# Kernel optimization log

Measured on AMD Instinct MI355X. Metric: run time of the kernel, lower is better.

Reference implementation:

```python
import jax, jax.numpy as jnp
import numpy as np

HID = 64
ENC_T = 20
DEC_T = 30


def lstm_cell(x, h, c, W_ih, W_hh, b_ih, b_hh):
    # PyTorch LSTMCell gate order: i, f, g, o
    gates = x @ W_ih.T + h @ W_hh.T + b_ih + b_hh  # [B, 4*HID]
    i, f, g, o = jnp.split(gates, 4, axis=-1)
    c_new = jax.nn.sigmoid(f) * c + jax.nn.sigmoid(i) * jnp.tanh(g)
    h_new = jax.nn.sigmoid(o) * jnp.tanh(c_new)
    return h_new, c_new


def setup_inputs() -> dict:
    key = jax.random.key(0)
    ks = jax.random.split(key, 11)
    B = 65536
    s_enc = 1.0 / np.sqrt(HID)
    u = lambda k, shape: jax.random.uniform(k, shape, jnp.float32, -s_enc, s_enc)
    return {
        "train_traj": jax.random.normal(ks[0], (B, ENC_T, 2), jnp.float32),
        "W_ih_enc": u(ks[1], (4 * HID, 2)),
        "W_hh_enc": u(ks[2], (4 * HID, HID)),
        "b_ih_enc": u(ks[3], (4 * HID,)),
        "b_hh_enc": u(ks[4], (4 * HID,)),
        "W_ih_dec": u(ks[5], (4 * HID, HID)),
        "W_hh_dec": u(ks[6], (4 * HID, HID)),
        "b_ih_dec": u(ks[7], (4 * HID,)),
        "b_hh_dec": u(ks[8], (4 * HID,)),
        "W_pos": u(ks[9], (2, HID)),
        "b_pos": u(ks[10], (2,)),
    }


def reference(train_traj, W_ih_enc, W_hh_enc, b_ih_enc, b_hh_enc,
              W_ih_dec, W_hh_dec, b_ih_dec, b_hh_dec, W_pos, b_pos):
    B = train_traj.shape[0]
    h0 = jnp.zeros((B, HID), train_traj.dtype)
    c0 = jnp.zeros((B, HID), train_traj.dtype)

    # Encoder: scan over the 20 time steps
    def enc_step(carry, x_t):
        h, c = carry
        h, c = lstm_cell(x_t, h, c, W_ih_enc, W_hh_enc, b_ih_enc, b_hh_enc)
        return (h, c), None

    xs = jnp.transpose(train_traj, (1, 0, 2))  # [T, B, 2]
    (h, c), _ = jax.lax.scan(enc_step, (h0, c0), xs)

    # Decoder: feed h back in as the input for 30 steps
    def dec_step(carry, _):
        h, c = carry
        h_new, c_new = lstm_cell(h, h, c, W_ih_dec, W_hh_dec, b_ih_dec, b_hh_dec)
        out = h_new @ W_pos.T + b_pos  # [B, 2]
        return (h_new, c_new), out

    (_, _), outs = jax.lax.scan(dec_step, (h, c), None, length=DEC_T)
    return jnp.transpose(outs, (1, 0, 2))  # [B, 30, 2]
```

## Files before the change

### kernel.cpp

```cpp
#include <hip/hip_runtime.h>

#define HID   64
#define ENC_T 20
#define DEC_T 30
#define ROWS  32
#define HS    72

typedef _Float16 f16;
typedef _Float16 f16x8 __attribute__((ext_vector_type(8)));
typedef _Float16 f16x4 __attribute__((ext_vector_type(4)));
typedef float  f32x4  __attribute__((ext_vector_type(4)));
typedef float  f32x2  __attribute__((ext_vector_type(2)));
typedef unsigned int   uint_t;

#if __has_builtin(__builtin_amdgcn_exp2f)
#define EXP2F(x) __builtin_amdgcn_exp2f(x)
#else
#define EXP2F(x) exp2f(x)
#endif
#if __has_builtin(__builtin_amdgcn_rcpf)
#define RCPF(x) __builtin_amdgcn_rcpf(x)
#else
#define RCPF(x) (1.0f / (x))
#endif

#define L2E 1.4426950408889634f

__device__ __forceinline__ f32x4 batch_inv4(float D0, float D1, float D2, float D3) {
    float m01 = D0 * D1;
    float m23 = D2 * D3;
    float r   = RCPF(m01 * m23);
    float r01 = r * m23;
    float r23 = r * m01;
    f32x4 o;
    o[0] = r01 * D1;
    o[1] = r01 * D0;
    o[2] = r23 * D3;
    o[3] = r23 * D2;
    return o;
}

__device__ __forceinline__ f16x8 load8h(const float* __restrict__ p, float s) {
    f16x8 r;
    #pragma unroll
    for (int u = 0; u < 8; ++u) r[u] = (f16)(p[u] * s);
    return r;
}

__global__ __launch_bounds__(256, 2)
void lstm_seq2seq(const float* __restrict__ traj,
                  const float* __restrict__ WihE, const float* __restrict__ WhhE,
                  const float* __restrict__ bihE, const float* __restrict__ bhhE,
                  const float* __restrict__ WihD, const float* __restrict__ WhhD,
                  const float* __restrict__ bihD, const float* __restrict__ bhhD,
                  const float* __restrict__ Wpos, const float* __restrict__ bpos,
                  float* __restrict__ out)
{
    __shared__ __align__(16) f16   sH[2][ROWS * HS];
    __shared__ __align__(16) f16x4 sXh[ROWS * ENC_T + ENC_T];
    __shared__ __align__(16) float sP[2][ROWS * 8];

    const int tid  = threadIdx.x;
    const int w    = tid >> 6;
    const int lane = tid & 63;
    const int col  = lane & 15;
    const int quad = lane >> 4;
    const int wg   = blockIdx.x;

    const float gsc[4] = { L2E, L2E, 2.0f * L2E, L2E };

    {
        const float* src = traj + (size_t)wg * (ROWS * ENC_T * 2);
        for (int p = tid; p < ROWS * ENC_T; p += 256) {
            f32x2 xp = *(const f32x2*)(src + 2 * p);
            f16 xh0 = (f16)xp[0], xh1 = (f16)xp[1];
            f16x4 v;
            v[0] = xh0; v[1] = xh1;
            v[2] = (f16)(xp[0] - (float)xh0);
            v[3] = (f16)(xp[1] - (float)xh1);
            sXh[p] = v;
        }
        if (tid < ENC_T) {
            f16x4 zz = {};
            sXh[ROWS * ENC_T + tid] = zz;
        }
    }
    {
        uint_t* hz = (uint_t*)&sH[0][0];
        for (int j = tid; j < ROWS * HS / 2; j += 256) hz[j] = 0;
    }

    f16x8 bw[4][3];
    #pragma unroll
    for (int j = 0; j < 4; ++j) {
        int g = 64 * j + 16 * w + col;
        #pragma unroll
        for (int kb = 0; kb < 2; ++kb)
            bw[j][kb] = load8h(WhhE + g * 64 + kb * 32 + quad * 8, gsc[j]);
        float w0 = WihE[g * 2 + 0] * gsc[j];
        float w1 = WihE[g * 2 + 1] * gsc[j];
        float bs = (bihE[g] + bhhE[g]) * gsc[j];
        f16 w0h = (f16)w0, w1h = (f16)w1, bh = (f16)bs;
        f16 w0l = (f16)(w0 - (float)w0h);
        f16 w1l = (f16)(w1 - (float)w1h);
        f16 bl  = (f16)(bs - (float)bh);
        f16x8 a2 = {};
        if (quad == 0) {
            a2[0] = w0h; a2[1] = w1h; a2[2] = w0l; a2[3] = w1l; a2[4] = bh; a2[5] = bl;
        }
        bw[j][2] = a2;
    }

    const uint_t onesd = (quad == 0) ? 0x3C003C00u : 0u;
    const int xbase0 = (quad == 0) ? (col      * ENC_T) : (ROWS * ENC_T);
    const int xbase1 = (quad == 0) ? ((col+16) * ENC_T) : (ROWS * ENC_T);
    const f32x4 z4 = { 0.f, 0.f, 0.f, 0.f };

    float c[2][4] = {{0.f,0.f,0.f,0.f},{0.f,0.f,0.f,0.f}};
    int buf = 0;

    __syncthreads();

    for (int t = 0; t < ENC_T; ++t) {
        #pragma unroll
        for (int g = 0; g < 2; ++g) {
            const int colg = col + 16 * g;
            union { f16x4 v; uint_t d[2]; } xfu;
            xfu.v = sXh[(g ? xbase1 : xbase0) + t];
            union { f16x8 v; uint_t d[4]; } b2u;
            b2u.d[0] = xfu.d[0];
            b2u.d[1] = xfu.d[1];
            b2u.d[2] = onesd;
            b2u.d[3] = 0;
            f16x8 b0 = *(const f16x8*)&sH[buf][colg * HS +  0 + quad * 8];
            f16x8 b1 = *(const f16x8*)&sH[buf][colg * HS + 32 + quad * 8];
            f32x4 acc[4];
            #pragma unroll
            for (int j = 0; j < 4; ++j) {
                acc[j] = __builtin_amdgcn_mfma_f32_16x16x32_f16(bw[j][2], b2u.v, z4, 0, 0, 0);
                acc[j] = __builtin_amdgcn_mfma_f32_16x16x32_f16(bw[j][0], b0, acc[j], 0, 0, 0);
                acc[j] = __builtin_amdgcn_mfma_f32_16x16x32_f16(bw[j][1], b1, acc[j], 0, 0, 0);
            }
            float so[4], cnv[4];
            #pragma unroll
            for (int r = 0; r < 4; ++r) {
                float ei = EXP2F(-acc[0][r]);
                float ef = EXP2F(-acc[1][r]);
                float eg = EXP2F(-acc[2][r]);
                float eo = EXP2F(-acc[3][r]);
                f32x4 inv = batch_inv4(1.0f + ei, 1.0f + ef, 1.0f + eg, 1.0f + eo);
                float tg = fmaf(2.0f, inv[2], -1.0f);
                float cn = fmaf(inv[1], c[g][r], inv[0] * tg);
                c[g][r] = cn;
                cnv[r] = cn;
                so[r] = inv[3];
            }
            float Dc[4];
            #pragma unroll
            for (int r = 0; r < 4; ++r) {
                float xs = cnv[r] * (-2.0f * L2E);
                xs = fminf(fmaxf(xs, -30.0f), 30.0f);
                Dc[r] = 1.0f + EXP2F(xs);
            }
            f32x4 invc = batch_inv4(Dc[0], Dc[1], Dc[2], Dc[3]);
            f16x4 hh;
            #pragma unroll
            for (int r = 0; r < 4; ++r) {
                float th = fmaf(2.0f, invc[r], -1.0f);
                float hn = so[r] * th;
                hh[r] = (f16)hn;
            }
            *(f16x4*)&sH[buf ^ 1][colg * HS + 16 * w + quad * 4] = hh;
        }
        __syncthreads();
        buf ^= 1;
    }

    f32x4 bD4[4];
    #pragma unroll
    for (int j = 0; j < 4; ++j) {
        int g = 64 * j + 16 * w + col;
        #pragma unroll
        for (int kb = 0; kb < 2; ++kb) {
            int off = g * 64 + kb * 32 + quad * 8;
            float tmp[8];
            #pragma unroll
            for (int u = 0; u < 8; ++u) tmp[u] = WihD[off + u] + WhhD[off + u];
            bw[j][kb] = load8h(tmp, gsc[j]);
        }
        #pragma unroll
        for (int r = 0; r < 4; ++r) {
            int gr = 64 * j + 16 * w + quad * 4 + r;
            bD4[j][r] = (bihD[gr] + bhhD[gr]) * gsc[j];
        }
    }

    float wpA[4], wpB[4];
    #pragma unroll
    for (int r = 0; r < 4; ++r) {
        int u = 16 * w + quad * 4 + r;
        wpA[r] = Wpos[u];
        wpB[r] = Wpos[64 + u];
    }
    const int   rrow  = w * 8 + (lane >> 1);
    const int   rcomp = lane & 1;
    const float bp    = bpos[rcomp];

    for (int t = 0; t < DEC_T; ++t) {
        #pragma unroll
        for (int g = 0; g < 2; ++g) {
            const int colg = col + 16 * g;
            f16x8 b0 = *(const f16x8*)&sH[buf][colg * HS +  0 + quad * 8];
            f16x8 b1 = *(const f16x8*)&sH[buf][colg * HS + 32 + quad * 8];
            f32x4 acc[4];
            #pragma unroll
            for (int j = 0; j < 4; ++j) {
                acc[j] = __builtin_amdgcn_mfma_f32_16x16x32_f16(bw[j][0], b0, bD4[j], 0, 0, 0);
                acc[j] = __builtin_amdgcn_mfma_f32_16x16x32_f16(bw[j][1], b1, acc[j], 0, 0, 0);
            }
            float so[4], cnv[4];
            #pragma unroll
            for (int r = 0; r < 4; ++r) {
                float ei = EXP2F(-acc[0][r]);
                float ef = EXP2F(-acc[1][r]);
                float eg = EXP2F(-acc[2][r]);
                float eo = EXP2F(-acc[3][r]);
                f32x4 inv = batch_inv4(1.0f + ei, 1.0f + ef, 1.0f + eg, 1.0f + eo);
                float tg = fmaf(2.0f, inv[2], -1.0f);
                float cn = fmaf(inv[1], c[g][r], inv[0] * tg);
                c[g][r] = cn;
                cnv[r] = cn;
                so[r] = inv[3];
            }
            float Dc[4];
            #pragma unroll
            for (int r = 0; r < 4; ++r) {
                float xs = cnv[r] * (-2.0f * L2E);
                xs = fminf(fmaxf(xs, -30.0f), 30.0f);
                Dc[r] = 1.0f + EXP2F(xs);
            }
            f32x4 invc = batch_inv4(Dc[0], Dc[1], Dc[2], Dc[3]);
            f16x4 hh;
            float p0 = 0.f, p1 = 0.f;
            #pragma unroll
            for (int r = 0; r < 4; ++r) {
                float th = fmaf(2.0f, invc[r], -1.0f);
                float hn = so[r] * th;
                p0 = fmaf(hn, wpA[r], p0);
                p1 = fmaf(hn, wpB[r], p1);
                hh[r] = (f16)hn;
            }
            *(f16x4*)&sH[buf ^ 1][colg * HS + 16 * w + quad * 4] = hh;
            p0 += __shfl_xor(p0, 16, 64);
            p0 += __shfl_xor(p0, 32, 64);
            p1 += __shfl_xor(p1, 16, 64);
            p1 += __shfl_xor(p1, 32, 64);
            if (quad == 0) {
                sP[buf ^ 1][colg * 8 + 0 + w] = p0;
                sP[buf ^ 1][colg * 8 + 4 + w] = p1;
            }
        }
        __syncthreads();
        buf ^= 1;
        if (lane < 16) {
            f32x4 v = *(const f32x4*)&sP[buf][rrow * 8 + rcomp * 4];
            float p = (v[0] + v[1]) + (v[2] + v[3]) + bp;
            out[(size_t)(wg * ROWS + rrow) * (DEC_T * 2) + t * 2 + rcomp] = p;
        }
    }
}

extern "C" void kernel_launch(void* const* d_in, const int* in_sizes, int n_in,
                              void* d_out, int out_size, void* d_ws, size_t ws_size,
                              hipStream_t stream) {
    const float* traj = (const float*)d_in[0];
    const float* WihE = (const float*)d_in[1];
    const float* WhhE = (const float*)d_in[2];
    const float* bihE = (const float*)d_in[3];
    const float* bhhE = (const float*)d_in[4];
    const float* WihD = (const float*)d_in[5];
    const float* WhhD = (const float*)d_in[6];
    const float* bihD = (const float*)d_in[7];
    const float* bhhD = (const float*)d_in[8];
    const float* Wpos = (const float*)d_in[9];
    const float* bpos = (const float*)d_in[10];
    float* out = (float*)d_out;

    const int B = in_sizes[0] / (ENC_T * 2);
    const int grid = B / ROWS;

    lstm_seq2seq<<<grid, 256, 0, stream>>>(traj, WihE, WhhE, bihE, bhhE,
                                           WihD, WhhD, bihD, bhhD, Wpos, bpos, out);
}
```

Measured before the change: 316.3 us.

## Compute position projection with MFMA from shared h and pack gate math into float2

The decoder's output projection h·W_pos^T, previously computed with per-lane FMAs, cross-lane shuffles and a shared-memory reduction buffer, is now done by wave 0 with four MFMAs over the h tile already loaded from shared memory. W_pos is split into hi/lo fp16 parts for accuracy. Each step's projection is issued one step late, with a final epilogue for the last step. The gate nonlinearities are also rewritten on float2 vectors to encourage packed FP32 instructions. This removes the shuffles, the sP buffer and the per-step reduction after the barrier, at the cost of extra MFMA work on wave 0 only, which unbalances the waves.

```diff
diff --git a/kernel.cpp b/kernel.cpp
--- a/kernel.cpp
+++ b/kernel.cpp
@@ -26,6 +26,24 @@
 
 #define L2E 1.4426950408889634f
 
+__device__ __forceinline__ f32x2 exp2_2(f32x2 x) {
+    f32x2 r; r[0] = EXP2F(x[0]); r[1] = EXP2F(x[1]); return r;
+}
+__device__ __forceinline__ void batch_inv4_pk(f32x2 D0, f32x2 D1, f32x2 D2, f32x2 D3,
+                                              f32x2& i0, f32x2& i1, f32x2& i2, f32x2& i3) {
+    f32x2 m01 = D0 * D1;
+    f32x2 m23 = D2 * D3;
+    f32x2 p   = m01 * m23;
+    f32x2 r;
+    r[0] = RCPF(p[0]);
+    r[1] = RCPF(p[1]);
+    f32x2 r01 = r * m23;
+    f32x2 r23 = r * m01;
+    i0 = r01 * D1;
+    i1 = r01 * D0;
+    i2 = r23 * D3;
+    i3 = r23 * D2;
+}
 __device__ __forceinline__ f32x4 batch_inv4(float D0, float D1, float D2, float D3) {
     float m01 = D0 * D1;
     float m23 = D2 * D3;
@@ -58,7 +76,6 @@
 {
     __shared__ __align__(16) f16   sH[2][ROWS * HS];
     __shared__ __align__(16) f16x4 sXh[ROWS * ENC_T + ENC_T];
-    __shared__ __align__(16) float sP[2][ROWS * 8];
 
     const int tid  = threadIdx.x;
     const int w    = tid >> 6;
@@ -116,7 +133,12 @@
     const int xbase1 = (quad == 0) ? ((col+16) * ENC_T) : (ROWS * ENC_T);
     const f32x4 z4 = { 0.f, 0.f, 0.f, 0.f };
 
-    float c[2][4] = {{0.f,0.f,0.f,0.f},{0.f,0.f,0.f,0.f}};
+    const f32x2 one2  = { 1.f, 1.f };
+    const f32x2 two2  = { 2.f, 2.f };
+    const f32x2 mone2 = { -1.f, -1.f };
+    const f32x2 msc2  = { -2.f * L2E, -2.f * L2E };
+
+    f32x2 c2[2][2] = {{{0.f,0.f},{0.f,0.f}},{{0.f,0.f},{0.f,0.f}}};
     int buf = 0;
 
     __syncthreads();
@@ -141,34 +163,39 @@
                 acc[j] = __builtin_amdgcn_mfma_f32_16x16x32_f16(bw[j][0], b0, acc[j], 0, 0, 0);
                 acc[j] = __builtin_amdgcn_mfma_f32_16x16x32_f16(bw[j][1], b1, acc[j], 0, 0, 0);
             }
-            float so[4], cnv[4];
-            #pragma unroll
-            for (int r = 0; r < 4; ++r) {
-                float ei = EXP2F(-acc[0][r]);
-                float ef = EXP2F(-acc[1][r]);
-                float eg = EXP2F(-acc[2][r]);
-                float eo = EXP2F(-acc[3][r]);
-                f32x4 inv = batch_inv4(1.0f + ei, 1.0f + ef, 1.0f + eg, 1.0f + eo);
-                float tg = fmaf(2.0f, inv[2], -1.0f);
-                float cn = fmaf(inv[1], c[g][r], inv[0] * tg);
-                c[g][r] = cn;
-                cnv[r] = cn;
-                so[r] = inv[3];
+            f32x2 so2[2], cn2[2];
+            #pragma unroll
+            for (int rp = 0; rp < 2; ++rp) {
+                f32x2 a0 = { acc[0][2*rp], acc[0][2*rp+1] };
+                f32x2 a1 = { acc[1][2*rp], acc[1][2*rp+1] };
+                f32x2 a2v = { acc[2][2*rp], acc[2][2*rp+1] };
+                f32x2 a3 = { acc[3][2*rp], acc[3][2*rp+1] };
+                f32x2 i0, i1, i2, i3;
+                batch_inv4_pk(exp2_2(-a0) + one2, exp2_2(-a1) + one2,
+                              exp2_2(-a2v) + one2, exp2_2(-a3) + one2,
+                              i0, i1, i2, i3);
+                f32x2 tg = __builtin_elementwise_fma(two2, i2, mone2);
+                f32x2 cn = __builtin_elementwise_fma(i1, c2[g][rp], i0 * tg);
+                c2[g][rp] = cn;
+                cn2[rp] = cn;
+                so2[rp] = i3;
             }
             float Dc[4];
             #pragma unroll
-            for (int r = 0; r < 4; ++r) {
-                float xs = cnv[r] * (-2.0f * L2E);
-                xs = fminf(fmaxf(xs, -30.0f), 30.0f);
-                Dc[r] = 1.0f + EXP2F(xs);
+            for (int rp = 0; rp < 2; ++rp) {
+                f32x2 xs = cn2[rp] * msc2;
+                Dc[2*rp+0] = 1.f + EXP2F(fminf(fmaxf(xs[0], -30.f), 30.f));
+                Dc[2*rp+1] = 1.f + EXP2F(fminf(fmaxf(xs[1], -30.f), 30.f));
             }
             f32x4 invc = batch_inv4(Dc[0], Dc[1], Dc[2], Dc[3]);
             f16x4 hh;
             #pragma unroll
-            for (int r = 0; r < 4; ++r) {
-                float th = fmaf(2.0f, invc[r], -1.0f);
-                float hn = so[r] * th;
-                hh[r] = (f16)hn;
+            for (int rp = 0; rp < 2; ++rp) {
+                f32x2 ic = { invc[2*rp], invc[2*rp+1] };
+                f32x2 th = __builtin_elementwise_fma(two2, ic, mone2);
+                f32x2 hn = so2[rp] * th;
+                hh[2*rp+0] = (f16)hn[0];
+                hh[2*rp+1] = (f16)hn[1];
             }
             *(f16x4*)&sH[buf ^ 1][colg * HS + 16 * w + quad * 4] = hh;
         }
@@ -195,16 +222,23 @@
         }
     }
 
-    float wpA[4], wpB[4];
+    f16x8 wpH[2], wpL[2];
     #pragma unroll
-    for (int r = 0; r < 4; ++r) {
-        int u = 16 * w + quad * 4 + r;
-        wpA[r] = Wpos[u];
-        wpB[r] = Wpos[64 + u];
-    }
-    const int   rrow  = w * 8 + (lane >> 1);
-    const int   rcomp = lane & 1;
-    const float bp    = bpos[rcomp];
+    for (int kb = 0; kb < 2; ++kb) {
+        f16x8 hv = {}, lv = {};
+        if (col < 2) {
+            #pragma unroll
+            for (int u = 0; u < 8; ++u) {
+                float v = Wpos[col * 64 + kb * 32 + quad * 8 + u];
+                f16 vh = (f16)v;
+                hv[u] = vh;
+                lv[u] = (f16)(v - (float)vh);
+            }
+        }
+        wpH[kb] = hv; wpL[kb] = lv;
+    }
+    f32x4 pinit = { 0.f, 0.f, 0.f, 0.f };
+    if (quad == 0) { pinit[0] = bpos[0]; pinit[1] = bpos[1]; }
 
     for (int t = 0; t < DEC_T; ++t) {
         #pragma unroll
@@ -212,60 +246,78 @@
             const int colg = col + 16 * g;
             f16x8 b0 = *(const f16x8*)&sH[buf][colg * HS +  0 + quad * 8];
             f16x8 b1 = *(const f16x8*)&sH[buf][colg * HS + 32 + quad * 8];
+            if (w == 0 && t > 0) {
+                f32x4 pc = pinit;
+                pc = __builtin_amdgcn_mfma_f32_16x16x32_f16(wpH[0], b0, pc, 0, 0, 0);
+                pc = __builtin_amdgcn_mfma_f32_16x16x32_f16(wpH[1], b1, pc, 0, 0, 0);
+                pc = __builtin_amdgcn_mfma_f32_16x16x32_f16(wpL[0], b0, pc, 0, 0, 0);
+                pc = __builtin_amdgcn_mfma_f32_16x16x32_f16(wpL[1], b1, pc, 0, 0, 0);
+                if (lane < 16) {
+                    f32x2 ov = { pc[0], pc[1] };
+                    *(f32x2*)&out[((size_t)(wg * ROWS + g * 16 + col)) * (DEC_T * 2) + (t - 1) * 2] = ov;
+                }
+            }
             f32x4 acc[4];
             #pragma unroll
             for (int j = 0; j < 4; ++j) {
                 acc[j] = __builtin_amdgcn_mfma_f32_16x16x32_f16(bw[j][0], b0, bD4[j], 0, 0, 0);
                 acc[j] = __builtin_amdgcn_mfma_f32_16x16x32_f16(bw[j][1], b1, acc[j], 0, 0, 0);
             }
-            float so[4], cnv[4];
-            #pragma unroll
-            for (int r = 0; r < 4; ++r) {
-                float ei = EXP2F(-acc[0][r]);
-                float ef = EXP2F(-acc[1][r]);
-                float eg = EXP2F(-acc[2][r]);
-                float eo = EXP2F(-acc[3][r]);
-                f32x4 inv = batch_inv4(1.0f + ei, 1.0f + ef, 1.0f + eg, 1.0f + eo);
-                float tg = fmaf(2.0f, inv[2], -1.0f);
-                float cn = fmaf(inv[1], c[g][r], inv[0] * tg);
-                c[g][r] = cn;
-                cnv[r] = cn;
-                so[r] = inv[3];
+            f32x2 so2[2], cn2[2];
+            #pragma unroll
+            for (int rp = 0; rp < 2; ++rp) {
+                f32x2 a0 = { acc[0][2*rp], acc[0][2*rp+1] };
+                f32x2 a1 = { acc[1][2*rp], acc[1][2*rp+1] };
+                f32x2 a2v = { acc[2][2*rp], acc[2][2*rp+1] };
+                f32x2 a3 = { acc[3][2*rp], acc[3][2*rp+1] };
+                f32x2 i0, i1, i2, i3;
+                batch_inv4_pk(exp2_2(-a0) + one2, exp2_2(-a1) + one2,
+                              exp2_2(-a2v) + one2, exp2_2(-a3) + one2,
+                              i0, i1, i2, i3);
+                f32x2 tg = __builtin_elementwise_fma(two2, i2, mone2);
+                f32x2 cn = __builtin_elementwise_fma(i1, c2[g][rp], i0 * tg);
+                c2[g][rp] = cn;
+                cn2[rp] = cn;
+                so2[rp] = i3;
             }
             float Dc[4];
             #pragma unroll
-            for (int r = 0; r < 4; ++r) {
-                float xs = cnv[r] * (-2.0f * L2E);
-                xs = fminf(fmaxf(xs, -30.0f), 30.0f);
-                Dc[r] = 1.0f + EXP2F(xs);
+            for (int rp = 0; rp < 2; ++rp) {
+                f32x2 xs = cn2[rp] * msc2;
+                Dc[2*rp+0] = 1.f + EXP2F(fminf(fmaxf(xs[0], -30.f), 30.f));
+                Dc[2*rp+1] = 1.f + EXP2F(fminf(fmaxf(xs[1], -30.f), 30.f));
             }
             f32x4 invc = batch_inv4(Dc[0], Dc[1], Dc[2], Dc[3]);
             f16x4 hh;
-            float p0 = 0.f, p1 = 0.f;
-            #pragma unroll
-            for (int r = 0; r < 4; ++r) {
-                float th = fmaf(2.0f, invc[r], -1.0f);
-                float hn = so[r] * th;
-                p0 = fmaf(hn, wpA[r], p0);
-                p1 = fmaf(hn, wpB[r], p1);
-                hh[r] = (f16)hn;
+            #pragma unroll
+            for (int rp = 0; rp < 2; ++rp) {
+                f32x2 ic = { invc[2*rp], invc[2*rp+1] };
+                f32x2 th = __builtin_elementwise_fma(two2, ic, mone2);
+                f32x2 hn = so2[rp] * th;
+                hh[2*rp+0] = (f16)hn[0];
+                hh[2*rp+1] = (f16)hn[1];
             }
             *(f16x4*)&sH[buf ^ 1][colg * HS + 16 * w + quad * 4] = hh;
-            p0 += __shfl_xor(p0, 16, 64);
-            p0 += __shfl_xor(p0, 32, 64);
-            p1 += __shfl_xor(p1, 16, 64);
-            p1 += __shfl_xor(p1, 32, 64);
-            if (quad == 0) {
-                sP[buf ^ 1][colg * 8 + 0 + w] = p0;
-                sP[buf ^ 1][colg * 8 + 4 + w] = p1;
-            }
         }
         __syncthreads();
         buf ^= 1;
-        if (lane < 16) {
-            f32x4 v = *(const f32x4*)&sP[buf][rrow * 8 + rcomp * 4];
-            float p = (v[0] + v[1]) + (v[2] + v[3]) + bp;
-            out[(size_t)(wg * ROWS + rrow) * (DEC_T * 2) + t * 2 + rcomp] = p;
+    }
+
+    if (w == 0) {
+        #pragma unroll
+        for (int g = 0; g < 2; ++g) {
+            const int colg = col + 16 * g;
+            f16x8 b0 = *(const f16x8*)&sH[buf][colg * HS +  0 + quad * 8];
+            f16x8 b1 = *(const f16x8*)&sH[buf][colg * HS + 32 + quad * 8];
+            f32x4 pc = pinit;
+            pc = __builtin_amdgcn_mfma_f32_16x16x32_f16(wpH[0], b0, pc, 0, 0, 0);
+            pc = __builtin_amdgcn_mfma_f32_16x16x32_f16(wpH[1], b1, pc, 0, 0, 0);
+            pc = __builtin_amdgcn_mfma_f32_16x16x32_f16(wpL[0], b0, pc, 0, 0, 0);
+            pc = __builtin_amdgcn_mfma_f32_16x16x32_f16(wpL[1], b1, pc, 0, 0, 0);
+            if (lane < 16) {
+                f32x2 ov = { pc[0], pc[1] };
+                *(f32x2*)&out[((size_t)(wg * ROWS + g * 16 + col)) * (DEC_T * 2) + (DEC_T - 1) * 2] = ov;
+            }
         }
     }
 }
```

After: 333.9 us. 5.5% more time.
